# Kernel tuning notes

Measured on AMD Instinct MI355X. Metric: run time of the kernel, lower is better.

Reference implementation:

```python
import jax, jax.numpy as jnp
import numpy as np

N = 50000
E = 800000
D = 128
NUM_GRAPHS = 64
NEG_SLOPE = 0.2


def _gat_conv(x, src, dst, W, a_src, a_dst, bias):
    """PyG GATConv with heads=1, concat=True. src/dst include self-loops."""
    h = x @ W                                  # [N, D_out]
    alpha_s = h @ a_src                        # [N]
    alpha_d = h @ a_dst                        # [N]
    e = alpha_s[src] + alpha_d[dst]            # [E_tot] edge scores
    e = jnp.where(e > 0, e, NEG_SLOPE * e)     # LeakyReLU(0.2)
    # numerically-stable softmax over incoming edges of each dst node
    m = jax.ops.segment_max(e, dst, num_segments=N)
    m = jnp.where(jnp.isfinite(m), m, 0.0)
    ex = jnp.exp(e - m[dst])
    s = jax.ops.segment_sum(ex, dst, num_segments=N)
    coef = ex / (s[dst] + 1e-16)               # [E_tot]
    msg = h[src] * coef[:, None]               # [E_tot, D_out] gathered messages
    out = jax.ops.segment_sum(msg, dst, num_segments=N)
    return out + bias


def setup_inputs() -> dict:
    key = jax.random.key(0)
    ks = jax.random.split(key, 12)
    x = jax.random.normal(ks[0], (N, D), dtype=jnp.float32)
    edge_index = jax.random.randint(ks[1], (2, E), 0, N, dtype=jnp.int64)
    batch = jnp.sort(jax.random.randint(ks[2], (N,), 0, NUM_GRAPHS, dtype=jnp.int64))
    g = 1.0 / np.sqrt(D)
    W1 = jax.random.normal(ks[3], (D, D), dtype=jnp.float32) * g
    as1 = jax.random.normal(ks[4], (D,), dtype=jnp.float32) * g
    ad1 = jax.random.normal(ks[5], (D,), dtype=jnp.float32) * g
    b1 = jnp.zeros((D,), dtype=jnp.float32)
    W2 = jax.random.normal(ks[6], (D, D), dtype=jnp.float32) * g
    as2 = jax.random.normal(ks[7], (D,), dtype=jnp.float32) * g
    ad2 = jax.random.normal(ks[8], (D,), dtype=jnp.float32) * g
    b2 = jnp.zeros((D,), dtype=jnp.float32)
    return {"x": x, "edge_index": edge_index, "batch": batch,
            "W1": W1, "as1": as1, "ad1": ad1, "b1": b1,
            "W2": W2, "as2": as2, "ad2": ad2, "b2": b2}


def reference(x, edge_index, batch, W1, as1, ad1, b1, W2, as2, ad2, b2):
    # PyG GATConv adds self-loops by default
    loops = jnp.arange(N, dtype=edge_index.dtype)
    src = jnp.concatenate([edge_index[0], loops])
    dst = jnp.concatenate([edge_index[1], loops])
    feats = _gat_conv(x, src, dst, W1, as1, ad1, b1)
    feats = _gat_conv(feats, src, dst, W2, as2, ad2, b2)
    # global mean pool over graphs in the batch
    sums = jax.ops.segment_sum(feats, batch, num_segments=NUM_GRAPHS)
    counts = jax.ops.segment_sum(jnp.ones((N,), feats.dtype), batch, num_segments=NUM_GRAPHS)
    pooled = sums / jnp.maximum(counts, 1.0)[:, None]
    return feats, pooled
```

## Files before the change

### kernel.cpp

```cpp
#include <hip/hip_runtime.h>

#define NN 50000
#define NE 800000
#define DIM 128
#define NG 64
#define ETOT (NE + NN)
#define NEG_SLOPE 0.2f
#define PB 200
#define MAXLG 8
#define NSH 8
#define SHW ((NN + NSH - 1) / NSH)
#define NB_SCAN ((NN + 255) / 256)
#define CAP 2048

typedef unsigned int uint32;
typedef unsigned short ushort;
typedef short bf16x8 __attribute__((ext_vector_type(8)));
typedef float f32x4 __attribute__((ext_vector_type(4)));

static __device__ __forceinline__ uint32 f2bf_pack(float lo, float hi) {
  uint32 a = __float_as_uint(lo), b = __float_as_uint(hi);
  a = (a + 0x7fffu + ((a >> 16) & 1u)) >> 16;
  b = (b + 0x7fffu + ((b >> 16) & 1u)) >> 16;
  return a | (b << 16);
}
static __device__ __forceinline__ ushort f2bf1(float x) {
  uint32 a = __float_as_uint(x);
  a = (a + 0x7fffu + ((a >> 16) & 1u)) >> 16;
  return (ushort)a;
}
static __device__ __forceinline__ float bf_lo(uint32 u) { return __uint_as_float(u << 16); }
static __device__ __forceinline__ float bf_hi(uint32 u) { return __uint_as_float(u & 0xffff0000u); }


__global__ __launch_bounds__(256) void k_init(const float* __restrict__ W1, const float* __restrict__ W2,
                                              ushort* __restrict__ wt1, ushort* __restrict__ wt2,
                                              int* deg, int* fill, float* pooled, float* cnt) {
  int i = blockIdx.x * 256 + threadIdx.x;
  if (i < NN) { deg[i] = 1; fill[i] = 1; }
  if (i < NG * DIM) pooled[i] = 0.f;
  if (i < NG) cnt[i] = 0.f;
  if (i < DIM * DIM) {
    int n = i >> 7, k = i & 127;
    wt1[i] = f2bf1(W1[k * DIM + n]);
    wt2[i] = f2bf1(W2[k * DIM + n]);
  }
}

__global__ __launch_bounds__(256) void k_count(const int* __restrict__ dst, int* __restrict__ deg) {
  int e = blockIdx.x * 256 + threadIdx.x;
  if (e < NE) atomicAdd(&deg[dst[e]], 1);
}


__global__ __launch_bounds__(256) void k_scan1(const int* __restrict__ deg, int* __restrict__ offs,
                                               int* __restrict__ bsum) {
  __shared__ int ws[4];
  const int i = blockIdx.x * 256 + threadIdx.x;
  const int lane = threadIdx.x & 63, wid = threadIdx.x >> 6;
  int x = (i < NN) ? deg[i] : 0;
#pragma unroll
  for (int off = 1; off < 64; off <<= 1) {
    int t = __shfl_up(x, off, 64);
    if (lane >= off) x += t;
  }
  if (lane == 63) ws[wid] = x;
  __syncthreads();
  int pre = 0;
#pragma unroll
  for (int j = 0; j < 3; ++j) if (j < wid) pre += ws[j];
  x += pre;
  if (i < NN) offs[i + 1] = x;
  if (threadIdx.x == 255) bsum[blockIdx.x] = x;
}

__global__ __launch_bounds__(256) void k_scan2(const int* __restrict__ bsum, int* __restrict__ bpre) {
  __shared__ int ws[4];
  const int b = threadIdx.x;
  const int lane = b & 63, wid = b >> 6;
  int v = (b < NB_SCAN) ? bsum[b] : 0;
  int x = v;
#pragma unroll
  for (int off = 1; off < 64; off <<= 1) {
    int t = __shfl_up(x, off, 64);
    if (lane >= off) x += t;
  }
  if (lane == 63) ws[wid] = x;
  __syncthreads();
  int pre = 0;
#pragma unroll
  for (int j = 0; j < 3; ++j) if (j < wid) pre += ws[j];
  x += pre;
  if (b < NB_SCAN) bpre[b] = x - v;
}

__global__ __launch_bounds__(256) void k_scan3(int* __restrict__ offs, const int* __restrict__ bpre,
                                               const int* __restrict__ deg, int* __restrict__ csr) {
  const int i = blockIdx.x * 256 + threadIdx.x;
  if (i < NN) {
    int v = offs[i + 1] + bpre[blockIdx.x];
    offs[i + 1] = v;
    csr[v - deg[i]] = i;
  }
  if (i == 0) offs[0] = 0;
}

__global__ __launch_bounds__(256) void k_scatter(const int* __restrict__ src, const int* __restrict__ dst,
                                                 const int* __restrict__ offs, int* __restrict__ fill,
                                                 int* __restrict__ csr) {
  const int r = blockIdx.x & (NSH - 1);
  const int bi = blockIdx.x >> 3;
  const int nb = gridDim.x >> 3;
  const int lo = r * SHW, hi = min(lo + SHW, NN);
  for (int e = bi * 256 + threadIdx.x; e < NE; e += nb * 256) {
    int d = dst[e];
    if (d >= lo && d < hi) {
      int p = offs[d] + atomicAdd(&fill[d], 1);
      csr[p] = src[e];
    }
  }
}


template <int A16>
__global__ __launch_bounds__(256) void k_mm(const void* __restrict__ Xv, const ushort* __restrict__ WT,
                                            const float* __restrict__ a_s, const float* __restrict__ a_d,
                                            uint32* __restrict__ H16,
                                            float* __restrict__ alpha_s, float* __restrict__ alpha_d, int n) {
  __shared__ __align__(16) ushort sWT[DIM * DIM];
  __shared__ __align__(16) ushort sA[64 * DIM];
  const int tid = threadIdx.x;
  const int row0 = blockIdx.x * 64;

  {
    const int nr = tid >> 1, h2 = tid & 1;
    const uint4* wp = (const uint4*)(WT + nr * DIM + h2 * 64);
#pragma unroll
    for (int i = 0; i < 8; ++i) {
      uint4 v = wp[i];
      int byte = nr * 256 + (((h2 * 128 + i * 16)) ^ ((nr & 7) << 4));
      *(uint4*)((char*)sWT + byte) = v;
    }
  }
  {
    const int r = tid >> 2, q = tid & 3;
    int rg = row0 + r; if (rg > n - 1) rg = n - 1;
    if (A16) {
      const uint4* xp = (const uint4*)((const uint32*)Xv + (size_t)rg * 64 + q * 16);
#pragma unroll
      for (int i = 0; i < 4; ++i) {
        uint4 pk = xp[i];
        int byte = r * 256 + ((q * 64 + i * 16) ^ ((r & 7) << 4));
        *(uint4*)((char*)sA + byte) = pk;
      }
    } else {
      const float4* xp = (const float4*)((const float*)Xv + (size_t)rg * DIM + q * 32);
#pragma unroll
      for (int i = 0; i < 4; ++i) {
        float4 v0 = xp[2 * i], v1 = xp[2 * i + 1];
        uint4 pk = make_uint4(f2bf_pack(v0.x, v0.y), f2bf_pack(v0.z, v0.w),
                              f2bf_pack(v1.x, v1.y), f2bf_pack(v1.z, v1.w));
        int byte = r * 256 + ((q * 64 + i * 16) ^ ((r & 7) << 4));
        *(uint4*)((char*)sA + byte) = pk;
      }
    }
  }
  __syncthreads();

  const int l = tid & 63, wv = tid >> 6;
  const int jr = l & 15, g = l >> 4;
  const int m0 = wv * 16;
  f32x4 acc[8];
#pragma unroll
  for (int nt = 0; nt < 8; ++nt) acc[nt] = (f32x4){0.f, 0.f, 0.f, 0.f};

  const int ra = m0 + jr;
  const int abase = ra * 256, aswz = (ra & 7) << 4;
  const int bswz = (jr & 7) << 4;
#pragma unroll
  for (int kk = 0; kk < 4; ++kk) {
    const int kb = kk * 64 + g * 16;
    bf16x8 af = *(const bf16x8*)((const char*)sA + abase + (kb ^ aswz));
#pragma unroll
    for (int nt = 0; nt < 8; ++nt) {
      bf16x8 bfg = *(const bf16x8*)((const char*)sWT + (nt * 16 + jr) * 256 + (kb ^ bswz));
      acc[nt] = __builtin_amdgcn_mfma_f32_16x16x32_bf16(af, bfg, acc[nt], 0, 0, 0);
    }
  }

  float asv[8], adv[8];
#pragma unroll
  for (int nt = 0; nt < 8; ++nt) { asv[nt] = a_s[nt * 16 + jr]; adv[nt] = a_d[nt * 16 + jr]; }
#pragma unroll
  for (int j = 0; j < 4; ++j) {
    float ps = 0.f, pd = 0.f;
#pragma unroll
    for (int nt = 0; nt < 8; ++nt) {
      ps = fmaf(acc[nt][j], asv[nt], ps);
      pd = fmaf(acc[nt][j], adv[nt], pd);
    }
#pragma unroll
    for (int off = 1; off < 16; off <<= 1) {
      ps += __shfl_xor(ps, off, 64);
      pd += __shfl_xor(pd, off, 64);
    }
    int r = row0 + m0 + g * 4 + j;
    if (jr == 0 && r < n) { alpha_s[r] = ps; alpha_d[r] = pd; }
  }

  ushort* sOut = sA;
#pragma unroll
  for (int nt = 0; nt < 8; ++nt)
#pragma unroll
    for (int j = 0; j < 4; ++j)
      sOut[(m0 + g * 4 + j) * DIM + nt * 16 + jr] = f2bf1(acc[nt][j]);
#pragma unroll
  for (int i = 0; i < 4; ++i) {
    int r = row0 + m0 + (l >> 4) + i * 4;
    uint4 v = *(const uint4*)((const char*)sOut + m0 * 256 + l * 16 + i * 1024);
    if (r < n) *(uint4*)(H16 + (size_t)(row0 + m0) * 64 + l * 4 + i * 256) = v;
  }
}


template <int STORE16>
__global__ __launch_bounds__(256) void k_sma(const int* __restrict__ offs, const int* __restrict__ csr,
                                             const float* __restrict__ alpha_s, const float* __restrict__ alpha_d,
                                             const uint32* __restrict__ H16, const float* __restrict__ bias,
                                             float* __restrict__ out, uint32* __restrict__ out16) {
  __shared__ int s_src[CAP];
  __shared__ float s_ex[CAP];
  __shared__ float s_inv[64];
  __shared__ int s_off[65];
  const int tid = threadIdx.x;
  const int n0 = blockIdx.x * 64;
  const int nn = min(64, NN - n0);
  if (tid <= nn) s_off[tid] = offs[n0 + tid];
  __syncthreads();
  const int ebeg = s_off[0];
  const int nE = s_off[nn] - ebeg;
  const int l = tid & 63, wv = tid >> 6;
  const float2 bb = *(const float2*)(bias + 2 * l);

  if (nE <= CAP) {
    for (int e = tid; e < nE; e += 256) {
      int sv = csr[ebeg + e];
      s_src[e] = sv;
      s_ex[e] = alpha_s[sv];
    }
    __syncthreads();
    {
      const int g = tid >> 4, l16 = tid & 15;
      for (int i = g; i < nn; i += 16) {
        const float ad = alpha_d[n0 + i];
        const int jb = s_off[i] - ebeg, je = s_off[i + 1] - ebeg;
        float m = -1e30f;
        for (int j = jb + l16; j < je; j += 16) {
          float sc = s_ex[j] + ad;
          sc = sc > 0.f ? sc : NEG_SLOPE * sc;
          m = fmaxf(m, sc);
        }
#pragma unroll
        for (int off = 1; off < 16; off <<= 1) m = fmaxf(m, __shfl_xor(m, off, 64));
        float ssum = 0.f;
        for (int j = jb + l16; j < je; j += 16) {
          float sc = s_ex[j] + ad;
          sc = sc > 0.f ? sc : NEG_SLOPE * sc;
          float ex = __expf(sc - m);
          s_ex[j] = ex;
          ssum += ex;
        }
#pragma unroll
        for (int off = 1; off < 16; off <<= 1) ssum += __shfl_xor(ssum, off, 64);
        if (l16 == 0) s_inv[i] = 1.f / (ssum + 1e-16f);
      }
    }
    __syncthreads();
    for (int i = wv; i < nn; i += 4) {
      const int jb = s_off[i] - ebeg, je = s_off[i + 1] - ebeg;
      float ax = 0.f, ay = 0.f;
      int j = jb;
      for (; j + 3 < je; j += 4) {
        int s0 = s_src[j], s1 = s_src[j + 1], s2 = s_src[j + 2], s3 = s_src[j + 3];
        float c0 = s_ex[j], c1 = s_ex[j + 1], c2 = s_ex[j + 2], c3 = s_ex[j + 3];
        uint32 v0 = H16[(size_t)s0 * 64 + l];
        uint32 v1 = H16[(size_t)s1 * 64 + l];
        uint32 v2 = H16[(size_t)s2 * 64 + l];
        uint32 v3 = H16[(size_t)s3 * 64 + l];
        ax = fmaf(c0, bf_lo(v0), ax); ay = fmaf(c0, bf_hi(v0), ay);
        ax = fmaf(c1, bf_lo(v1), ax); ay = fmaf(c1, bf_hi(v1), ay);
        ax = fmaf(c2, bf_lo(v2), ax); ay = fmaf(c2, bf_hi(v2), ay);
        ax = fmaf(c3, bf_lo(v3), ax); ay = fmaf(c3, bf_hi(v3), ay);
      }
      for (; j < je; ++j) {
        int s0 = s_src[j]; float c0 = s_ex[j];
        uint32 v0 = H16[(size_t)s0 * 64 + l];
        ax = fmaf(c0, bf_lo(v0), ax); ay = fmaf(c0, bf_hi(v0), ay);
      }
      const float inv = s_inv[i];
      const float ox = ax * inv + bb.x, oy = ay * inv + bb.y;
      const int node = n0 + i;
      if (STORE16) out16[(size_t)node * 64 + l] = f2bf_pack(ox, oy);
      else *(float2*)(out + (size_t)node * DIM + 2 * l) = make_float2(ox, oy);
    }
  } else {
    for (int i = wv; i < nn; i += 4) {
      const int node = n0 + i;
      const int bg = offs[node], eg = offs[node + 1];
      const float ad = alpha_d[node];
      float m = -1e30f;
      for (int jj = bg + l; jj < eg; jj += 64) {
        float sc = alpha_s[csr[jj]] + ad;
        sc = sc > 0.f ? sc : NEG_SLOPE * sc;
        m = fmaxf(m, sc);
      }
#pragma unroll
      for (int off = 1; off < 64; off <<= 1) m = fmaxf(m, __shfl_xor(m, off, 64));
      float ax = 0.f, ay = 0.f, ssum = 0.f;
      for (int base = bg; base < eg; base += 64) {
        int cnt = min(64, eg - base);
        int sv = 0; float ex = 0.f;
        if (l < cnt) {
          sv = csr[base + l];
          float sc = alpha_s[sv] + ad;
          sc = sc > 0.f ? sc : NEG_SLOPE * sc;
          ex = __expf(sc - m);
        }
        ssum += ex;
        for (int jj = 0; jj < cnt; ++jj) {
          int s0 = __shfl(sv, jj, 64); float c0 = __shfl(ex, jj, 64);
          uint32 v0 = H16[(size_t)s0 * 64 + l];
          ax = fmaf(c0, bf_lo(v0), ax); ay = fmaf(c0, bf_hi(v0), ay);
        }
      }
#pragma unroll
      for (int off = 1; off < 64; off <<= 1) ssum += __shfl_xor(ssum, off, 64);
      const float inv = 1.f / (ssum + 1e-16f);
      const float ox = ax * inv + bb.x, oy = ay * inv + bb.y;
      if (STORE16) out16[(size_t)node * 64 + l] = f2bf_pack(ox, oy);
      else *(float2*)(out + (size_t)node * DIM + 2 * l) = make_float2(ox, oy);
    }
  }
}


__global__ __launch_bounds__(256) void k_pool_partial(const float* __restrict__ feats,
                                                      const int* __restrict__ batch,
                                                      float* __restrict__ pooled, float* __restrict__ cnt) {
  __shared__ float acc[4][MAXLG][DIM];
  __shared__ float lcnt[4][MAXLG];
  const int tid = threadIdx.x;
  const int wid = tid >> 6, l = tid & 63;
  for (int i = tid; i < 4 * MAXLG * DIM; i += 256) ((float*)acc)[i] = 0.f;
  if (tid < 4 * MAXLG) ((float*)lcnt)[tid] = 0.f;
  __syncthreads();

  const int chunk = (NN + PB - 1) / PB;
  const int beg = blockIdx.x * chunk;
  const int end = min(beg + chunk, NN);
  const int g0 = (beg < NN) ? batch[beg] : 0;

  for (int node = beg + wid; node < end; node += 4) {
    int lg = batch[node] - g0;
    float2 v = *(const float2*)(feats + (size_t)node * DIM + 2 * l);
    if (lg < MAXLG) {
      acc[wid][lg][2 * l] += v.x;
      acc[wid][lg][2 * l + 1] += v.y;
      if (l == 0) lcnt[wid][lg] += 1.f;
    } else {
      atomicAdd(&pooled[(g0 + lg) * DIM + 2 * l], v.x);
      atomicAdd(&pooled[(g0 + lg) * DIM + 2 * l + 1], v.y);
      if (l == 0) atomicAdd(&cnt[g0 + lg], 1.f);
    }
  }
  __syncthreads();

  for (int i = tid; i < MAXLG * DIM; i += 256) {
    int lg = i >> 7, d = i & (DIM - 1);
    float s = acc[0][lg][d] + acc[1][lg][d] + acc[2][lg][d] + acc[3][lg][d];
    if (s != 0.f) atomicAdd(&pooled[(g0 + lg) * DIM + d], s);
  }
  if (tid < MAXLG) {
    float s = lcnt[0][tid] + lcnt[1][tid] + lcnt[2][tid] + lcnt[3][tid];
    if (s != 0.f) atomicAdd(&cnt[g0 + tid], s);
  }
}

__global__ __launch_bounds__(256) void k_pool_norm(float* pooled, const float* __restrict__ cnt) {
  int i = blockIdx.x * 256 + threadIdx.x;
  if (i < NG * DIM) pooled[i] /= fmaxf(cnt[i >> 7], 1.f);
}


static inline size_t pad256(size_t x) { return (x + 255) & ~(size_t)255; }

extern "C" void kernel_launch(void* const* d_in, const int* in_sizes, int n_in,
                              void* d_out, int out_size, void* d_ws, size_t ws_size,
                              hipStream_t stream) {
  const float* x   = (const float*)d_in[0];
  const int* ei    = (const int*)d_in[1];
  const int* batch = (const int*)d_in[2];
  const float* W1  = (const float*)d_in[3];
  const float* as1 = (const float*)d_in[4];
  const float* ad1 = (const float*)d_in[5];
  const float* b1  = (const float*)d_in[6];
  const float* W2  = (const float*)d_in[7];
  const float* as2 = (const float*)d_in[8];
  const float* ad2 = (const float*)d_in[9];
  const float* b2  = (const float*)d_in[10];

  float* out_feats = (float*)d_out;
  float* pooled    = out_feats + (size_t)NN * DIM;

  const int* src = ei;
  const int* dst = ei + NE;

  char* w = (char*)d_ws;
  uint32* h16 = (uint32*)w;   w += pad256((size_t)NN * 64 * 4);
  uint32* f116 = (uint32*)w;  w += pad256((size_t)NN * 64 * 4);
  float* alpha_s = (float*)w; w += pad256((size_t)NN * 4);
  float* alpha_d = (float*)w; w += pad256((size_t)NN * 4);
  int* deg  = (int*)w;        w += pad256((size_t)NN * 4);
  int* offs = (int*)w;        w += pad256((size_t)(NN + 1) * 4);
  int* fill = (int*)w;        w += pad256((size_t)NN * 4);
  int* csr  = (int*)w;        w += pad256((size_t)ETOT * 4);
  float* cnt  = (float*)w;    w += pad256((size_t)NG * 4);
  int* bsum = (int*)w;        w += pad256((size_t)NB_SCAN * 4);
  int* bpre = (int*)w;        w += pad256((size_t)NB_SCAN * 4);
  ushort* wt1 = (ushort*)w;   w += pad256((size_t)DIM * DIM * 2);
  ushort* wt2 = (ushort*)w;   w += pad256((size_t)DIM * DIM * 2);

  const int NB_N = (NN + 255) / 256;
  const int NB_E = (NE + 255) / 256;
  const int NB_A = (NN + 63) / 64;
  const int NB_G = (NN + 63) / 64;
  const int NB_SC = 1024;

  k_init<<<NB_N, 256, 0, stream>>>(W1, W2, wt1, wt2, deg, fill, pooled, cnt);
  k_count<<<NB_E, 256, 0, stream>>>(dst, deg);
  k_scan1<<<NB_SCAN, 256, 0, stream>>>(deg, offs, bsum);
  k_scan2<<<1, 256, 0, stream>>>(bsum, bpre);
  k_scan3<<<NB_SCAN, 256, 0, stream>>>(offs, bpre, deg, csr);
  k_scatter<<<NB_SC, 256, 0, stream>>>(src, dst, offs, fill, csr);

  k_mm<0><<<NB_G, 256, 0, stream>>>(x, wt1, as1, ad1, h16, alpha_s, alpha_d, NN);
  k_sma<1><<<NB_A, 256, 0, stream>>>(offs, csr, alpha_s, alpha_d, h16, b1, nullptr, f116);

  k_mm<1><<<NB_G, 256, 0, stream>>>(f116, wt2, as2, ad2, h16, alpha_s, alpha_d, NN);
  k_sma<0><<<NB_A, 256, 0, stream>>>(offs, csr, alpha_s, alpha_d, h16, b2, out_feats, nullptr);

  k_pool_partial<<<PB, 256, 0, stream>>>(out_feats, batch, pooled, cnt);
  k_pool_norm<<<(NG * DIM + 255) / 256, 256, 0, stream>>>(pooled, cnt);
}
```

Before: 248.0 us.

## Shrink aggregation blocks to four nodes with one wave per node

The softmax-aggregate kernel now handles 4 destination nodes per block instead of 64, with each wave owning one node for the max, the exp-sum and the gather. Source index and score are packed into one int2 shared array, and the shared capacity drops to 512 edges. The aim is more blocks and less shared memory per block for higher occupancy, plus fewer block-wide barriers and better load balance across nodes. In exchange there are many more blocks, each paying to load offsets, and the softmax now uses 64-lane reductions instead of 16-lane ones.

New measurement: 223.9 us. 9.7% less time.

```diff
diff --git a/kernel.cpp b/kernel.cpp
--- a/kernel.cpp
+++ b/kernel.cpp
@@ -11,7 +11,7 @@
 #define NSH 8
 #define SHW ((NN + NSH - 1) / NSH)
 #define NB_SCAN ((NN + 255) / 256)
-#define CAP 2048
+#define CAP 512
 
 typedef unsigned int uint32;
 typedef unsigned short ushort;
@@ -228,119 +228,103 @@
                                              const float* __restrict__ alpha_s, const float* __restrict__ alpha_d,
                                              const uint32* __restrict__ H16, const float* __restrict__ bias,
                                              float* __restrict__ out, uint32* __restrict__ out16) {
-  __shared__ int s_src[CAP];
-  __shared__ float s_ex[CAP];
-  __shared__ float s_inv[64];
-  __shared__ int s_off[65];
+  __shared__ int2 s_pair[CAP];
+  __shared__ int s_off[5];
   const int tid = threadIdx.x;
-  const int n0 = blockIdx.x * 64;
-  const int nn = min(64, NN - n0);
-  if (tid <= nn) s_off[tid] = offs[n0 + tid];
+  const int n0 = blockIdx.x * 4;
+  if (tid <= 4) s_off[tid] = offs[n0 + tid];
   __syncthreads();
   const int ebeg = s_off[0];
-  const int nE = s_off[nn] - ebeg;
+  const int nE = s_off[4] - ebeg;
   const int l = tid & 63, wv = tid >> 6;
+  const int node = n0 + wv;
   const float2 bb = *(const float2*)(bias + 2 * l);
+  float ax = 0.f, ay = 0.f, inv;
 
   if (nE <= CAP) {
     for (int e = tid; e < nE; e += 256) {
       int sv = csr[ebeg + e];
-      s_src[e] = sv;
-      s_ex[e] = alpha_s[sv];
+      s_pair[e] = make_int2(sv, __float_as_int(alpha_s[sv]));
     }
     __syncthreads();
-    {
-      const int g = tid >> 4, l16 = tid & 15;
-      for (int i = g; i < nn; i += 16) {
-        const float ad = alpha_d[n0 + i];
-        const int jb = s_off[i] - ebeg, je = s_off[i + 1] - ebeg;
-        float m = -1e30f;
-        for (int j = jb + l16; j < je; j += 16) {
-          float sc = s_ex[j] + ad;
-          sc = sc > 0.f ? sc : NEG_SLOPE * sc;
-          m = fmaxf(m, sc);
-        }
-#pragma unroll
-        for (int off = 1; off < 16; off <<= 1) m = fmaxf(m, __shfl_xor(m, off, 64));
-        float ssum = 0.f;
-        for (int j = jb + l16; j < je; j += 16) {
-          float sc = s_ex[j] + ad;
-          sc = sc > 0.f ? sc : NEG_SLOPE * sc;
-          float ex = __expf(sc - m);
-          s_ex[j] = ex;
-          ssum += ex;
-        }
-#pragma unroll
-        for (int off = 1; off < 16; off <<= 1) ssum += __shfl_xor(ssum, off, 64);
-        if (l16 == 0) s_inv[i] = 1.f / (ssum + 1e-16f);
+    const int jb = s_off[wv] - ebeg, je = s_off[wv + 1] - ebeg;
+    const float ad = alpha_d[node];
+    float m = -1e30f;
+    for (int j = jb + l; j < je; j += 64) {
+      float sc = __int_as_float(s_pair[j].y) + ad;
+      sc = sc > 0.f ? sc : NEG_SLOPE * sc;
+      m = fmaxf(m, sc);
+    }
+#pragma unroll
+    for (int off = 1; off < 64; off <<= 1) m = fmaxf(m, __shfl_xor(m, off, 64));
+    float ssum = 0.f;
+    for (int j = jb + l; j < je; j += 64) {
+      float sc = __int_as_float(s_pair[j].y) + ad;
+      sc = sc > 0.f ? sc : NEG_SLOPE * sc;
+      float ex = __expf(sc - m);
+      s_pair[j].y = __float_as_int(ex);
+      ssum += ex;
+    }
+#pragma unroll
+    for (int off = 1; off < 64; off <<= 1) ssum += __shfl_xor(ssum, off, 64);
+    inv = 1.f / (ssum + 1e-16f);
+
+    int j = jb;
+    for (; j + 3 < je; j += 4) {
+      int2 p0 = s_pair[j], p1 = s_pair[j + 1], p2 = s_pair[j + 2], p3 = s_pair[j + 3];
+      uint32 v0 = H16[(size_t)p0.x * 64 + l];
+      uint32 v1 = H16[(size_t)p1.x * 64 + l];
+      uint32 v2 = H16[(size_t)p2.x * 64 + l];
+      uint32 v3 = H16[(size_t)p3.x * 64 + l];
+      float c0 = __int_as_float(p0.y), c1 = __int_as_float(p1.y);
+      float c2 = __int_as_float(p2.y), c3 = __int_as_float(p3.y);
+      ax = fmaf(c0, bf_lo(v0), ax); ay = fmaf(c0, bf_hi(v0), ay);
+      ax = fmaf(c1, bf_lo(v1), ax); ay = fmaf(c1, bf_hi(v1), ay);
+      ax = fmaf(c2, bf_lo(v2), ax); ay = fmaf(c2, bf_hi(v2), ay);
+      ax = fmaf(c3, bf_lo(v3), ax); ay = fmaf(c3, bf_hi(v3), ay);
+    }
+    for (; j < je; ++j) {
+      int2 p0 = s_pair[j];
+      uint32 v0 = H16[(size_t)p0.x * 64 + l];
+      float c0 = __int_as_float(p0.y);
+      ax = fmaf(c0, bf_lo(v0), ax); ay = fmaf(c0, bf_hi(v0), ay);
+    }
+  } else {
+    const int bg = offs[node], eg = offs[node + 1];
+    const float ad = alpha_d[node];
+    float m = -1e30f;
+    for (int jj = bg + l; jj < eg; jj += 64) {
+      float sc = alpha_s[csr[jj]] + ad;
+      sc = sc > 0.f ? sc : NEG_SLOPE * sc;
+      m = fmaxf(m, sc);
+    }
+#pragma unroll
+    for (int off = 1; off < 64; off <<= 1) m = fmaxf(m, __shfl_xor(m, off, 64));
+    float ssum = 0.f;
+    for (int base = bg; base < eg; base += 64) {
+      int cnt = min(64, eg - base);
+      int sv = 0; float ex = 0.f;
+      if (l < cnt) {
+        sv = csr[base + l];
+        float sc = alpha_s[sv] + ad;
+        sc = sc > 0.f ? sc : NEG_SLOPE * sc;
+        ex = __expf(sc - m);
       }
-    }
-    __syncthreads();
-    for (int i = wv; i < nn; i += 4) {
-      const int jb = s_off[i] - ebeg, je = s_off[i + 1] - ebeg;
-      float ax = 0.f, ay = 0.f;
-      int j = jb;
-      for (; j + 3 < je; j += 4) {
-        int s0 = s_src[j], s1 = s_src[j + 1], s2 = s_src[j + 2], s3 = s_src[j + 3];
-        float c0 = s_ex[j], c1 = s_ex[j + 1], c2 = s_ex[j + 2], c3 = s_ex[j + 3];
-        uint32 v0 = H16[(size_t)s0 * 64 + l];
-        uint32 v1 = H16[(size_t)s1 * 64 + l];
-        uint32 v2 = H16[(size_t)s2 * 64 + l];
-        uint32 v3 = H16[(size_t)s3 * 64 + l];
-        ax = fmaf(c0, bf_lo(v0), ax); ay = fmaf(c0, bf_hi(v0), ay);
-        ax = fmaf(c1, bf_lo(v1), ax); ay = fmaf(c1, bf_hi(v1), ay);
-        ax = fmaf(c2, bf_lo(v2), ax); ay = fmaf(c2, bf_hi(v2), ay);
-        ax = fmaf(c3, bf_lo(v3), ax); ay = fmaf(c3, bf_hi(v3), ay);
-      }
-      for (; j < je; ++j) {
-        int s0 = s_src[j]; float c0 = s_ex[j];
+      ssum += ex;
+      for (int jj = 0; jj < cnt; ++jj) {
+        int s0 = __shfl(sv, jj, 64); float c0 = __shfl(ex, jj, 64);
         uint32 v0 = H16[(size_t)s0 * 64 + l];
         ax = fmaf(c0, bf_lo(v0), ax); ay = fmaf(c0, bf_hi(v0), ay);
       }
-      const float inv = s_inv[i];
-      const float ox = ax * inv + bb.x, oy = ay * inv + bb.y;
-      const int node = n0 + i;
-      if (STORE16) out16[(size_t)node * 64 + l] = f2bf_pack(ox, oy);
-      else *(float2*)(out + (size_t)node * DIM + 2 * l) = make_float2(ox, oy);
-    }
-  } else {
-    for (int i = wv; i < nn; i += 4) {
-      const int node = n0 + i;
-      const int bg = offs[node], eg = offs[node + 1];
-      const float ad = alpha_d[node];
-      float m = -1e30f;
-      for (int jj = bg + l; jj < eg; jj += 64) {
-        float sc = alpha_s[csr[jj]] + ad;
-        sc = sc > 0.f ? sc : NEG_SLOPE * sc;
-        m = fmaxf(m, sc);
-      }
-#pragma unroll
-      for (int off = 1; off < 64; off <<= 1) m = fmaxf(m, __shfl_xor(m, off, 64));
-      float ax = 0.f, ay = 0.f, ssum = 0.f;
-      for (int base = bg; base < eg; base += 64) {
-        int cnt = min(64, eg - base);
-        int sv = 0; float ex = 0.f;
-        if (l < cnt) {
-          sv = csr[base + l];
-          float sc = alpha_s[sv] + ad;
-          sc = sc > 0.f ? sc : NEG_SLOPE * sc;
-          ex = __expf(sc - m);
-        }
-        ssum += ex;
-        for (int jj = 0; jj < cnt; ++jj) {
-          int s0 = __shfl(sv, jj, 64); float c0 = __shfl(ex, jj, 64);
-          uint32 v0 = H16[(size_t)s0 * 64 + l];
-          ax = fmaf(c0, bf_lo(v0), ax); ay = fmaf(c0, bf_hi(v0), ay);
-        }
-      }
-#pragma unroll
-      for (int off = 1; off < 64; off <<= 1) ssum += __shfl_xor(ssum, off, 64);
-      const float inv = 1.f / (ssum + 1e-16f);
-      const float ox = ax * inv + bb.x, oy = ay * inv + bb.y;
-      if (STORE16) out16[(size_t)node * 64 + l] = f2bf_pack(ox, oy);
-      else *(float2*)(out + (size_t)node * DIM + 2 * l) = make_float2(ox, oy);
-    }
-  }
+    }
+#pragma unroll
+    for (int off = 1; off < 64; off <<= 1) ssum += __shfl_xor(ssum, off, 64);
+    inv = 1.f / (ssum + 1e-16f);
+  }
+
+  const float ox = ax * inv + bb.x, oy = ay * inv + bb.y;
+  if (STORE16) out16[(size_t)node * 64 + l] = f2bf_pack(ox, oy);
+  else *(float2*)(out + (size_t)node * DIM + 2 * l) = make_float2(ox, oy);
 }
 
 
@@ -432,7 +416,7 @@
 
   const int NB_N = (NN + 255) / 256;
   const int NB_E = (NE + 255) / 256;
-  const int NB_A = (NN + 63) / 64;
+  const int NB_A = NN / 4;
   const int NB_G = (NN + 63) / 64;
   const int NB_SC = 1024;
 
```
